# Optimization experiments

Measured on AMD Instinct MI355X. Metric: run time of the kernel, lower is better.

The kernel has to match this reference:

```python
import jax, jax.numpy as jnp
import numpy as np

THR = 0.2          # config['thr']
BORDER = 2         # config['border_rm']
H0C, W0C = 60, 80  # coarse grid of image0 (L = 4800)
H1C, W1C = 60, 80  # coarse grid of image1 (S = 4800)
TEMP_INIT = 10.0


def _border_mask():
    # valid (non-border) positions of the [h0,w0,h1,w1] grid, flattened to [L,S]
    def ok(n):
        a = jnp.arange(n)
        return (a >= BORDER) & (a < n - BORDER)
    m = (ok(H0C)[:, None, None, None] & ok(W0C)[None, :, None, None]
         & ok(H1C)[None, None, :, None] & ok(W1C)[None, None, None, :])
    return m.reshape(H0C * W0C, H1C * W1C)


def setup_inputs() -> dict:
    key = jax.random.key(0)
    k0, k1 = jax.random.split(key)
    feat_c0 = jax.random.normal(k0, (2, 4800, 256), dtype=jnp.float32)
    feat_c1 = jax.random.normal(k1, (2, 4800, 256), dtype=jnp.float32)
    temperature = jnp.asarray(TEMP_INIT, dtype=jnp.float32)
    return {"feat_c0": feat_c0, "feat_c1": feat_c1, "temperature": temperature}


def reference(feat_c0, feat_c1, temperature):
    C = feat_c0.shape[-1]
    inv_sqrt_c = 1.0 / float(C) ** 0.5
    f0 = feat_c0 * inv_sqrt_c
    f1 = feat_c1 * inv_sqrt_c
    # dense similarity GEMM: [N,L,S]
    sim = jnp.einsum('nlc,nsc->nls', f0, f1) * temperature
    # dual softmax -> confidence matrix
    conf = jax.nn.softmax(sim, axis=1) * jax.nn.softmax(sim, axis=2)
    # threshold + border removal (mask_border with b=BORDER)
    mask = (conf > THR) & _border_mask()[None]
    # mutual nearest neighbor
    mutual = (mask
              & (conf == conf.max(axis=2, keepdims=True))
              & (conf == conf.max(axis=1, keepdims=True)))
    # dense mconf map: conf at selected matches, 0 elsewhere (fixed-shape
    # equivalent of the b_ids/i_ids/j_ids nonzero extraction)
    mconf = jnp.where(mutual, conf, jnp.zeros((), conf.dtype))
    return conf, mconf
```

## Files before the change

kernel.cpp:

```cpp
#include <hip/hip_runtime.h>

#define L 4800
#define CH 256
#define NB 2
#define TT 38

typedef float f32x4 __attribute__((ext_vector_type(4)));
typedef _Float16 h16;
typedef _Float16 h16x4 __attribute__((ext_vector_type(4)));
typedef _Float16 h16x8 __attribute__((ext_vector_type(8)));

__global__ __launch_bounds__(256) void convert_init(
    const float* __restrict__ f0, const float* __restrict__ f1,
    h16* __restrict__ A, h16* __restrict__ B,
    float* __restrict__ rowsum, float* __restrict__ colsum,
    unsigned* __restrict__ colmax, unsigned* __restrict__ cand_cnt)
{
    int idx = blockIdx.x * 256 + threadIdx.x;
    if (idx < NB * L) { rowsum[idx] = 0.f; colsum[idx] = 0.f; colmax[idx] = 0u; }
    if (idx == 0) cand_cnt[0] = 0u;
    if (idx >= NB * L * CH / 4) return;
    f32x4 a = ((const f32x4*)f0)[idx];
    f32x4 b = ((const f32x4*)f1)[idx];
    h16x4 ah, bh;
#pragma unroll
    for (int k = 0; k < 4; ++k) { ah[k] = (h16)a[k]; bh[k] = (h16)b[k]; }
    ((h16x4*)A)[idx] = ah;
    ((h16x4*)B)[idx] = bh;
}

__global__ __launch_bounds__(256) void gemm_exp(
    const h16* __restrict__ A, const h16* __restrict__ B,
    const float* __restrict__ temp,
    h16* __restrict__ E, float* __restrict__ rowsum, float* __restrict__ colsum)
{
    __shared__ __align__(16) h16 As[128 * 32];
    __shared__ __align__(16) h16 Bs[128 * 32];
    int bid = blockIdx.x;
    int n = bid / (TT * TT);
    int t = bid % (TT * TT);
    int tm = (t / TT) * 128;
    int tn = (t % TT) * 128;
    const h16* Ab = A + (long)n * L * CH;
    const h16* Bb = B + (long)n * L * CH;
    int tid = threadIdx.x;
    int lane = tid & 63;
    int w = tid >> 6;
    int wr = (w >> 1) * 64;
    int wc = (w & 1) * 64;

    f32x4 acc[4][4] = {};

    int lrow = lane >> 2;
    int kc8 = (lane & 3) * 8;

    for (int k0 = 0; k0 < CH; k0 += 32) {
        __syncthreads();
#pragma unroll
        for (int j = 0; j < 2; ++j) {
            int c = w * 2 + j;
            int row = c * 16 + lrow;
            int ga = tm + row; ga = ga > L - 1 ? L - 1 : ga;
            int gb = tn + row; gb = gb > L - 1 ? L - 1 : gb;
            __builtin_amdgcn_global_load_lds(
                (const __attribute__((address_space(1))) void*)(Ab + (long)ga * CH + k0 + kc8),
                (__attribute__((address_space(3))) void*)(As + c * 512), 16, 0, 0);
            __builtin_amdgcn_global_load_lds(
                (const __attribute__((address_space(1))) void*)(Bb + (long)gb * CH + k0 + kc8),
                (__attribute__((address_space(3))) void*)(Bs + c * 512), 16, 0, 0);
        }
        __syncthreads();

        h16x8 af[4], bf[4];
        int klo = (lane >> 4) * 8;
        int ra = wr + (lane & 15);
        int rb = wc + (lane & 15);
#pragma unroll
        for (int m = 0; m < 4; ++m) af[m] = *(const h16x8*)&As[(ra + m * 16) * 32 + klo];
#pragma unroll
        for (int nf = 0; nf < 4; ++nf) bf[nf] = *(const h16x8*)&Bs[(rb + nf * 16) * 32 + klo];
#pragma unroll
        for (int m = 0; m < 4; ++m)
#pragma unroll
            for (int nf = 0; nf < 4; ++nf)
                acc[m][nf] = __builtin_amdgcn_mfma_f32_16x16x32_f16(af[m], bf[nf], acc[m][nf], 0, 0, 0);
    }

    float scale = temp[0] * (1.0f / 256.0f);
    float rpart[4][4];
#pragma unroll
    for (int m = 0; m < 4; ++m)
#pragma unroll
        for (int j = 0; j < 4; ++j) rpart[m][j] = 0.f;
    float cpart[4] = {0.f, 0.f, 0.f, 0.f};
    int row0 = tm + wr + ((lane >> 4) * 4);
    int col0 = tn + wc + (lane & 15);
#pragma unroll
    for (int m = 0; m < 4; ++m) {
#pragma unroll
        for (int nf = 0; nf < 4; ++nf) {
#pragma unroll
            for (int j = 0; j < 4; ++j) {
                int rr = row0 + m * 16 + j;
                int cc = col0 + nf * 16;
                float e = 0.f;
                if (rr < L && cc < L) {
                    e = __expf(acc[m][nf][j] * scale);
                    E[((long)n * L + rr) * L + cc] = (h16)e;
                }
                rpart[m][j] += e;
                cpart[nf] += e;
            }
        }
    }
#pragma unroll
    for (int m = 0; m < 4; ++m)
#pragma unroll
        for (int j = 0; j < 4; ++j) {
            float v = rpart[m][j];
            v += __shfl_xor(v, 1); v += __shfl_xor(v, 2);
            v += __shfl_xor(v, 4); v += __shfl_xor(v, 8);
            if ((lane & 15) == 0) {
                int rr = row0 + m * 16 + j;
                if (rr < L) atomicAdd(&rowsum[n * L + rr], v);
            }
        }
#pragma unroll
    for (int nf = 0; nf < 4; ++nf) {
        float v = cpart[nf];
        v += __shfl_xor(v, 16); v += __shfl_xor(v, 32);
        if ((lane >> 4) == 0) {
            int cc = col0 + nf * 16;
            if (cc < L) atomicAdd(&colsum[n * L + cc], v);
        }
    }
}

__global__ void inv_kernel(const float* rowsum, const float* colsum, float* inv_rs, float* inv_cs) {
    int i = blockIdx.x * 256 + threadIdx.x;
    if (i < NB * L) { inv_rs[i] = 1.0f / rowsum[i]; inv_cs[i] = 1.0f / colsum[i]; }
}

__global__ __launch_bounds__(256) void conf_row(
    const h16* __restrict__ E, const float* __restrict__ inv_rs, const float* __restrict__ inv_cs,
    float* __restrict__ conf, float* __restrict__ rowmax,
    float* __restrict__ mzero,
    unsigned* __restrict__ cand, unsigned* __restrict__ cand_cnt, unsigned cand_cap)
{
    int b = blockIdx.x;
    int n = b / L;
    const h16x8* E8 = (const h16x8*)(E + (long)b * L);
    const f32x4* IC4 = (const f32x4*)(inv_cs + n * L);
    float* Crow = conf + (long)b * L;
    float irs = inv_rs[b];
    int tid = threadIdx.x;
    float m = 0.f;
    for (int i = tid; i < L / 8; i += 256) {
        h16x8 e8 = E8[i];
        f32x4 ic0 = IC4[2 * i], ic1 = IC4[2 * i + 1];
        f32x4 c0, c1;
#pragma unroll
        for (int k = 0; k < 4; ++k) {
            float e = (float)e8[k];
            float tt = (e * e) * irs;
            c0[k] = tt * ic0[k];
            m = fmaxf(m, c0[k]);
        }
#pragma unroll
        for (int k = 0; k < 4; ++k) {
            float e = (float)e8[4 + k];
            float tt = (e * e) * irs;
            c1[k] = tt * ic1[k];
            m = fmaxf(m, c1[k]);
        }
        *(f32x4*)&Crow[i * 8] = c0;
        *(f32x4*)&Crow[i * 8 + 4] = c1;
#pragma unroll
        for (int k = 0; k < 4; ++k) {
            if (c0[k] > 0.2f) {
                unsigned pos = atomicAdd(cand_cnt, 1u);
                if (pos < cand_cap) cand[pos] = (unsigned)b * L + (unsigned)(i * 8 + k);
            }
            if (c1[k] > 0.2f) {
                unsigned pos = atomicAdd(cand_cnt, 1u);
                if (pos < cand_cap) cand[pos] = (unsigned)b * L + (unsigned)(i * 8 + 4 + k);
            }
        }
    }
    if (mzero) {
        f32x4* M4 = (f32x4*)(mzero + (long)b * L);
        f32x4 z = {0.f, 0.f, 0.f, 0.f};
        for (int i = tid; i < L / 4; i += 256) M4[i] = z;
    }
#pragma unroll
    for (int off = 1; off < 64; off <<= 1) m = fmaxf(m, __shfl_xor(m, off));
    __shared__ float sm[4];
    int lane = tid & 63, wv = tid >> 6;
    if (lane == 0) sm[wv] = m;
    __syncthreads();
    if (tid == 0) rowmax[b] = fmaxf(fmaxf(sm[0], sm[1]), fmaxf(sm[2], sm[3]));
}

__global__ __launch_bounds__(256) void col_max(
    const h16* __restrict__ E, const float* __restrict__ inv_rs, const float* __restrict__ inv_cs,
    unsigned* __restrict__ colmax)
{
    int bx = blockIdx.x;
    int rc = bx & 31;
    int cc = (bx >> 5) % 19;
    int n = bx / (19 * 32);
    int col = cc * 256 + threadIdx.x;
    if (col >= L) return;
    const h16* p = E + ((long)n * L + rc * 150) * L + col;
    const float* irs = inv_rs + n * L + rc * 150;
    float m = 0.f;
    for (int i = 0; i < 150; ++i) {
        float e = (float)(*p);
        float tt = (e * e) * irs[i];
        m = fmaxf(m, tt);
        p += L;
    }
    float v = m * inv_cs[n * L + col];
    atomicMax(&colmax[n * L + col], __float_as_uint(v));
}

__global__ __launch_bounds__(256) void fill_zero(f32x4* __restrict__ p, long n4) {
    long i = (long)blockIdx.x * 256 + threadIdx.x;
    long stride = (long)gridDim.x * 256;
    f32x4 z = {0.f, 0.f, 0.f, 0.f};
    for (; i < n4; i += stride) p[i] = z;
}

__global__ __launch_bounds__(256) void cand_kernel(
    const unsigned* __restrict__ cand_cnt, const unsigned* __restrict__ cand, unsigned cand_cap,
    const float* __restrict__ conf, const float* __restrict__ rowmax,
    const unsigned* __restrict__ colmax, float* __restrict__ mconf)
{
    unsigned cnt = cand_cnt[0];
    if (cnt > cand_cap) cnt = cand_cap;
    for (unsigned i = blockIdx.x * 256 + threadIdx.x; i < cnt; i += gridDim.x * 256) {
        unsigned idx = cand[i];
        unsigned b = idx / L, s = idx % L;
        unsigned n = b / L, l = b % L;
        int h0 = l / 80, w0 = l % 80;
        int h1 = s / 80, w1 = s % 80;
        bool ok = (h0 >= 2) && (h0 < 58) && (w0 >= 2) && (w0 < 78)
               && (h1 >= 2) && (h1 < 58) && (w1 >= 2) && (w1 < 78);
        float c = conf[idx];
        if (ok && c == rowmax[b] && c == __uint_as_float(colmax[n * L + s]))
            mconf[idx] = c;
    }
}

extern "C" void kernel_launch(void* const* d_in, const int* in_sizes, int n_in,
                              void* d_out, int out_size, void* d_ws, size_t ws_size,
                              hipStream_t stream)
{
    const float* f0 = (const float*)d_in[0];
    const float* f1 = (const float*)d_in[1];
    const float* temp = (const float*)d_in[2];

    float* conf  = (float*)d_out;
    float* mconf = conf + (long)NB * L * L;

    h16* Abf = (h16*)d_out;
    h16* Bbf = (h16*)((char*)d_out + 8u * 1024u * 1024u);

    float* rowsum = (float*)d_ws;
    float* colsum = rowsum + NB * L;
    float* inv_rs = colsum + NB * L;
    float* inv_cs = inv_rs + NB * L;
    float* rowmax = inv_cs + NB * L;
    unsigned* colmax = (unsigned*)(rowmax + NB * L);
    unsigned* cand_cnt = colmax + NB * L;
    unsigned* cand = cand_cnt + 1;
    const unsigned cand_cap = 1u << 20;
    size_t stats_end = (size_t)((char*)(cand + cand_cap) - (char*)d_ws);
    size_t E_off = (stats_end + 255) & ~(size_t)255;
    size_t E_bytes = (size_t)NB * L * L * 2;
    bool E_in_ws = ws_size >= E_off + E_bytes;
    h16* E = E_in_ws ? (h16*)((char*)d_ws + E_off) : (h16*)mconf;

    convert_init<<<(NB * L * CH / 4 + 255) / 256, 256, 0, stream>>>(
        f0, f1, Abf, Bbf, rowsum, colsum, colmax, cand_cnt);
    gemm_exp<<<NB * TT * TT, 256, 0, stream>>>(Abf, Bbf, temp, E, rowsum, colsum);
    inv_kernel<<<(NB * L + 255) / 256, 256, 0, stream>>>(rowsum, colsum, inv_rs, inv_cs);
    conf_row<<<NB * L, 256, 0, stream>>>(E, inv_rs, inv_cs, conf, rowmax,
                                         E_in_ws ? mconf : (float*)nullptr,
                                         cand, cand_cnt, cand_cap);
    col_max<<<NB * 19 * 32, 256, 0, stream>>>(E, inv_rs, inv_cs, colmax);
    if (!E_in_ws)
        fill_zero<<<2048, 256, 0, stream>>>((f32x4*)mconf, (long)NB * L * L / 4);
    cand_kernel<<<128, 256, 0, stream>>>(cand_cnt, cand, cand_cap, conf, rowmax, colmax, mconf);
}
```

Baseline: 531.8 us.

## Recompute GEMM in a second pass instead of storing and rereading exp matrix

Replaces the materialized fp16 exp matrix with two GEMM passes. The first computes only row and column exp sums into per-tile partials, with no atomics. The second recomputes the GEMM, writes conf directly, zeroes mconf, and records per-tile row and column maxima. A row-skipping mconf kernel replaces the candidate list and atomics. This trades extra GEMM compute for removing a large intermediate write and read plus the separate column-max scan.

```diff
diff --git a/kernel.cpp b/kernel.cpp
--- a/kernel.cpp
+++ b/kernel.cpp
@@ -4,21 +4,19 @@
 #define CH 256
 #define NB 2
 #define TT 38
+#define NBL (NB * L)
+#define THRF 0.2f
 
 typedef float f32x4 __attribute__((ext_vector_type(4)));
 typedef _Float16 h16;
 typedef _Float16 h16x4 __attribute__((ext_vector_type(4)));
 typedef _Float16 h16x8 __attribute__((ext_vector_type(8)));
 
-__global__ __launch_bounds__(256) void convert_init(
+__global__ __launch_bounds__(256) void convert_kernel(
     const float* __restrict__ f0, const float* __restrict__ f1,
-    h16* __restrict__ A, h16* __restrict__ B,
-    float* __restrict__ rowsum, float* __restrict__ colsum,
-    unsigned* __restrict__ colmax, unsigned* __restrict__ cand_cnt)
+    h16* __restrict__ A, h16* __restrict__ B)
 {
     int idx = blockIdx.x * 256 + threadIdx.x;
-    if (idx < NB * L) { rowsum[idx] = 0.f; colsum[idx] = 0.f; colmax[idx] = 0u; }
-    if (idx == 0) cand_cnt[0] = 0u;
     if (idx >= NB * L * CH / 4) return;
     f32x4 a = ((const f32x4*)f0)[idx];
     f32x4 b = ((const f32x4*)f1)[idx];
@@ -29,13 +27,15 @@
     ((h16x4*)B)[idx] = bh;
 }
 
-__global__ __launch_bounds__(256) void gemm_exp(
+__global__ __launch_bounds__(256) void gemm_pass1(
     const h16* __restrict__ A, const h16* __restrict__ B,
     const float* __restrict__ temp,
-    h16* __restrict__ E, float* __restrict__ rowsum, float* __restrict__ colsum)
+    float* __restrict__ rs_part, float* __restrict__ cs_part)
 {
     __shared__ __align__(16) h16 As[128 * 32];
     __shared__ __align__(16) h16 Bs[128 * 32];
+    __shared__ float rp_lds[128][2];
+    __shared__ float cp_lds[128][2];
     int bid = blockIdx.x;
     int n = bid / (TT * TT);
     int t = bid % (TT * TT);
@@ -50,7 +50,6 @@
     int wc = (w & 1) * 64;
 
     f32x4 acc[4][4] = {};
-
     int lrow = lane >> 2;
     int kc8 = (lane & 3) * 8;
 
@@ -96,23 +95,18 @@
     int row0 = tm + wr + ((lane >> 4) * 4);
     int col0 = tn + wc + (lane & 15);
 #pragma unroll
-    for (int m = 0; m < 4; ++m) {
-#pragma unroll
-        for (int nf = 0; nf < 4; ++nf) {
+    for (int m = 0; m < 4; ++m)
+#pragma unroll
+        for (int nf = 0; nf < 4; ++nf)
 #pragma unroll
             for (int j = 0; j < 4; ++j) {
                 int rr = row0 + m * 16 + j;
                 int cc = col0 + nf * 16;
                 float e = 0.f;
-                if (rr < L && cc < L) {
-                    e = __expf(acc[m][nf][j] * scale);
-                    E[((long)n * L + rr) * L + cc] = (h16)e;
-                }
+                if (rr < L && cc < L) e = __expf(acc[m][nf][j] * scale);
                 rpart[m][j] += e;
                 cpart[nf] += e;
             }
-        }
-    }
 #pragma unroll
     for (int m = 0; m < 4; ++m)
 #pragma unroll
@@ -120,135 +114,204 @@
             float v = rpart[m][j];
             v += __shfl_xor(v, 1); v += __shfl_xor(v, 2);
             v += __shfl_xor(v, 4); v += __shfl_xor(v, 8);
-            if ((lane & 15) == 0) {
-                int rr = row0 + m * 16 + j;
-                if (rr < L) atomicAdd(&rowsum[n * L + rr], v);
-            }
+            if ((lane & 15) == 0)
+                rp_lds[wr + (lane >> 4) * 4 + m * 16 + j][w & 1] = v;
         }
 #pragma unroll
     for (int nf = 0; nf < 4; ++nf) {
         float v = cpart[nf];
         v += __shfl_xor(v, 16); v += __shfl_xor(v, 32);
-        if ((lane >> 4) == 0) {
-            int cc = col0 + nf * 16;
-            if (cc < L) atomicAdd(&colsum[n * L + cc], v);
-        }
-    }
-}
-
-__global__ void inv_kernel(const float* rowsum, const float* colsum, float* inv_rs, float* inv_cs) {
+        if (lane < 16)
+            cp_lds[wc + lane + nf * 16][w >> 1] = v;
+    }
+    __syncthreads();
+    if (tid < 128) {
+        int rr = tm + tid;
+        if (rr < L)
+            rs_part[(long)(t % TT) * NBL + n * L + rr] = rp_lds[tid][0] + rp_lds[tid][1];
+    } else {
+        int c2 = tid - 128;
+        int cc = tn + c2;
+        if (cc < L)
+            cs_part[(long)(t / TT) * NBL + n * L + cc] = cp_lds[c2][0] + cp_lds[c2][1];
+    }
+}
+
+__global__ __launch_bounds__(256) void reduce_inv(
+    const float* __restrict__ rs_part, const float* __restrict__ cs_part,
+    float* __restrict__ inv_rs, float* __restrict__ inv_cs)
+{
     int i = blockIdx.x * 256 + threadIdx.x;
-    if (i < NB * L) { inv_rs[i] = 1.0f / rowsum[i]; inv_cs[i] = 1.0f / colsum[i]; }
-}
-
-__global__ __launch_bounds__(256) void conf_row(
-    const h16* __restrict__ E, const float* __restrict__ inv_rs, const float* __restrict__ inv_cs,
-    float* __restrict__ conf, float* __restrict__ rowmax,
-    float* __restrict__ mzero,
-    unsigned* __restrict__ cand, unsigned* __restrict__ cand_cnt, unsigned cand_cap)
+    if (i < NBL) {
+        float s = 0.f;
+        for (int t = 0; t < TT; ++t) s += rs_part[(long)t * NBL + i];
+        inv_rs[i] = 1.0f / s;
+    } else if (i < 2 * NBL) {
+        int b = i - NBL;
+        float s = 0.f;
+        for (int t = 0; t < TT; ++t) s += cs_part[(long)t * NBL + b];
+        inv_cs[b] = 1.0f / s;
+    }
+}
+
+__global__ __launch_bounds__(256) void gemm_pass2(
+    const h16* __restrict__ A, const h16* __restrict__ B,
+    const float* __restrict__ temp,
+    const float* __restrict__ inv_rs, const float* __restrict__ inv_cs,
+    float* __restrict__ conf, float* __restrict__ mconf,
+    float* __restrict__ rm_part, float* __restrict__ cm_part)
+{
+    __shared__ __align__(16) h16 As[128 * 32];
+    __shared__ __align__(16) h16 Bs[128 * 32];
+    __shared__ float rp_lds[128][2];
+    __shared__ float cp_lds[128][2];
+    int bid = blockIdx.x;
+    int n = bid / (TT * TT);
+    int t = bid % (TT * TT);
+    int tm = (t / TT) * 128;
+    int tn = (t % TT) * 128;
+    const h16* Ab = A + (long)n * L * CH;
+    const h16* Bb = B + (long)n * L * CH;
+    int tid = threadIdx.x;
+    int lane = tid & 63;
+    int w = tid >> 6;
+    int wr = (w >> 1) * 64;
+    int wc = (w & 1) * 64;
+
+    f32x4 acc[4][4] = {};
+    int lrow = lane >> 2;
+    int kc8 = (lane & 3) * 8;
+
+    for (int k0 = 0; k0 < CH; k0 += 32) {
+        __syncthreads();
+#pragma unroll
+        for (int j = 0; j < 2; ++j) {
+            int c = w * 2 + j;
+            int row = c * 16 + lrow;
+            int ga = tm + row; ga = ga > L - 1 ? L - 1 : ga;
+            int gb = tn + row; gb = gb > L - 1 ? L - 1 : gb;
+            __builtin_amdgcn_global_load_lds(
+                (const __attribute__((address_space(1))) void*)(Ab + (long)ga * CH + k0 + kc8),
+                (__attribute__((address_space(3))) void*)(As + c * 512), 16, 0, 0);
+            __builtin_amdgcn_global_load_lds(
+                (const __attribute__((address_space(1))) void*)(Bb + (long)gb * CH + k0 + kc8),
+                (__attribute__((address_space(3))) void*)(Bs + c * 512), 16, 0, 0);
+        }
+        __syncthreads();
+
+        h16x8 af[4], bf[4];
+        int klo = (lane >> 4) * 8;
+        int ra = wr + (lane & 15);
+        int rb = wc + (lane & 15);
+#pragma unroll
+        for (int m = 0; m < 4; ++m) af[m] = *(const h16x8*)&As[(ra + m * 16) * 32 + klo];
+#pragma unroll
+        for (int nf = 0; nf < 4; ++nf) bf[nf] = *(const h16x8*)&Bs[(rb + nf * 16) * 32 + klo];
+#pragma unroll
+        for (int m = 0; m < 4; ++m)
+#pragma unroll
+            for (int nf = 0; nf < 4; ++nf)
+                acc[m][nf] = __builtin_amdgcn_mfma_f32_16x16x32_f16(af[m], bf[nf], acc[m][nf], 0, 0, 0);
+    }
+
+    float scale = temp[0] * (1.0f / 256.0f);
+    int row0 = tm + wr + ((lane >> 4) * 4);
+    int col0 = tn + wc + (lane & 15);
+    float ics[4];
+#pragma unroll
+    for (int nf = 0; nf < 4; ++nf) {
+        int cc = col0 + nf * 16;
+        ics[nf] = (cc < L) ? inv_cs[n * L + cc] : 0.f;
+    }
+    float cmax[4] = {0.f, 0.f, 0.f, 0.f};
+#pragma unroll
+    for (int m = 0; m < 4; ++m)
+#pragma unroll
+        for (int j = 0; j < 4; ++j) {
+            int rr = row0 + m * 16 + j;
+            float irs_v = (rr < L) ? inv_rs[n * L + rr] : 0.f;
+            float rm = 0.f;
+#pragma unroll
+            for (int nf = 0; nf < 4; ++nf) {
+                int cc = col0 + nf * 16;
+                if (rr < L && cc < L) {
+                    float e = __expf(acc[m][nf][j] * scale);
+                    float c = (e * e) * irs_v * ics[nf];
+                    conf[((long)n * L + rr) * L + cc] = c;
+                    rm = fmaxf(rm, c);
+                    cmax[nf] = fmaxf(cmax[nf], c);
+                }
+            }
+            rm = fmaxf(rm, __shfl_xor(rm, 1)); rm = fmaxf(rm, __shfl_xor(rm, 2));
+            rm = fmaxf(rm, __shfl_xor(rm, 4)); rm = fmaxf(rm, __shfl_xor(rm, 8));
+            if ((lane & 15) == 0)
+                rp_lds[wr + (lane >> 4) * 4 + m * 16 + j][w & 1] = rm;
+        }
+#pragma unroll
+    for (int nf = 0; nf < 4; ++nf) {
+        float v = cmax[nf];
+        v = fmaxf(v, __shfl_xor(v, 16)); v = fmaxf(v, __shfl_xor(v, 32));
+        if (lane < 16)
+            cp_lds[wc + lane + nf * 16][w >> 1] = v;
+    }
+    __syncthreads();
+    if (tid < 128) {
+        int rr = tm + tid;
+        if (rr < L)
+            rm_part[(long)(t % TT) * NBL + n * L + rr] = fmaxf(rp_lds[tid][0], rp_lds[tid][1]);
+    } else {
+        int c2 = tid - 128;
+        int cc = tn + c2;
+        if (cc < L)
+            cm_part[(long)(t / TT) * NBL + n * L + cc] = fmaxf(cp_lds[c2][0], cp_lds[c2][1]);
+    }
+
+    f32x4 z = {0.f, 0.f, 0.f, 0.f};
+    for (int i = tid; i < 128 * 32; i += 256) {
+        int r = i >> 5;
+        int cv = (i & 31) * 4;
+        int rr = tm + r, cc = tn + cv;
+        if (rr < L && cc + 3 < L)
+            *(f32x4*)&mconf[((long)n * L + rr) * L + cc] = z;
+    }
+}
+
+__global__ __launch_bounds__(256) void reduce_max(
+    const float* __restrict__ rm_part, const float* __restrict__ cm_part,
+    float* __restrict__ rowmaxf, float* __restrict__ colmaxf)
+{
+    int i = blockIdx.x * 256 + threadIdx.x;
+    if (i < NBL) {
+        float m = 0.f;
+        for (int t = 0; t < TT; ++t) m = fmaxf(m, rm_part[(long)t * NBL + i]);
+        rowmaxf[i] = m;
+    } else if (i < 2 * NBL) {
+        int b = i - NBL;
+        float m = 0.f;
+        for (int t = 0; t < TT; ++t) m = fmaxf(m, cm_part[(long)t * NBL + b]);
+        colmaxf[b] = m;
+    }
+}
+
+__global__ __launch_bounds__(256) void mconf_rows(
+    const float* __restrict__ conf, const float* __restrict__ rowmaxf,
+    const float* __restrict__ colmaxf, float* __restrict__ mconf)
 {
     int b = blockIdx.x;
+    float rmax = rowmaxf[b];
+    if (!(rmax > THRF)) return;
+    int l = b % L;
+    int h0 = l / 80, w0 = l % 80;
+    if (!((h0 >= 2) && (h0 < 58) && (w0 >= 2) && (w0 < 78))) return;
     int n = b / L;
-    const h16x8* E8 = (const h16x8*)(E + (long)b * L);
-    const f32x4* IC4 = (const f32x4*)(inv_cs + n * L);
-    float* Crow = conf + (long)b * L;
-    float irs = inv_rs[b];
-    int tid = threadIdx.x;
-    float m = 0.f;
-    for (int i = tid; i < L / 8; i += 256) {
-        h16x8 e8 = E8[i];
-        f32x4 ic0 = IC4[2 * i], ic1 = IC4[2 * i + 1];
-        f32x4 c0, c1;
-#pragma unroll
-        for (int k = 0; k < 4; ++k) {
-            float e = (float)e8[k];
-            float tt = (e * e) * irs;
-            c0[k] = tt * ic0[k];
-            m = fmaxf(m, c0[k]);
-        }
-#pragma unroll
-        for (int k = 0; k < 4; ++k) {
-            float e = (float)e8[4 + k];
-            float tt = (e * e) * irs;
-            c1[k] = tt * ic1[k];
-            m = fmaxf(m, c1[k]);
-        }
-        *(f32x4*)&Crow[i * 8] = c0;
-        *(f32x4*)&Crow[i * 8 + 4] = c1;
-#pragma unroll
-        for (int k = 0; k < 4; ++k) {
-            if (c0[k] > 0.2f) {
-                unsigned pos = atomicAdd(cand_cnt, 1u);
-                if (pos < cand_cap) cand[pos] = (unsigned)b * L + (unsigned)(i * 8 + k);
-            }
-            if (c1[k] > 0.2f) {
-                unsigned pos = atomicAdd(cand_cnt, 1u);
-                if (pos < cand_cap) cand[pos] = (unsigned)b * L + (unsigned)(i * 8 + 4 + k);
-            }
-        }
-    }
-    if (mzero) {
-        f32x4* M4 = (f32x4*)(mzero + (long)b * L);
-        f32x4 z = {0.f, 0.f, 0.f, 0.f};
-        for (int i = tid; i < L / 4; i += 256) M4[i] = z;
-    }
-#pragma unroll
-    for (int off = 1; off < 64; off <<= 1) m = fmaxf(m, __shfl_xor(m, off));
-    __shared__ float sm[4];
-    int lane = tid & 63, wv = tid >> 6;
-    if (lane == 0) sm[wv] = m;
-    __syncthreads();
-    if (tid == 0) rowmax[b] = fmaxf(fmaxf(sm[0], sm[1]), fmaxf(sm[2], sm[3]));
-}
-
-__global__ __launch_bounds__(256) void col_max(
-    const h16* __restrict__ E, const float* __restrict__ inv_rs, const float* __restrict__ inv_cs,
-    unsigned* __restrict__ colmax)
-{
-    int bx = blockIdx.x;
-    int rc = bx & 31;
-    int cc = (bx >> 5) % 19;
-    int n = bx / (19 * 32);
-    int col = cc * 256 + threadIdx.x;
-    if (col >= L) return;
-    const h16* p = E + ((long)n * L + rc * 150) * L + col;
-    const float* irs = inv_rs + n * L + rc * 150;
-    float m = 0.f;
-    for (int i = 0; i < 150; ++i) {
-        float e = (float)(*p);
-        float tt = (e * e) * irs[i];
-        m = fmaxf(m, tt);
-        p += L;
-    }
-    float v = m * inv_cs[n * L + col];
-    atomicMax(&colmax[n * L + col], __float_as_uint(v));
-}
-
-__global__ __launch_bounds__(256) void fill_zero(f32x4* __restrict__ p, long n4) {
-    long i = (long)blockIdx.x * 256 + threadIdx.x;
-    long stride = (long)gridDim.x * 256;
-    f32x4 z = {0.f, 0.f, 0.f, 0.f};
-    for (; i < n4; i += stride) p[i] = z;
-}
-
-__global__ __launch_bounds__(256) void cand_kernel(
-    const unsigned* __restrict__ cand_cnt, const unsigned* __restrict__ cand, unsigned cand_cap,
-    const float* __restrict__ conf, const float* __restrict__ rowmax,
-    const unsigned* __restrict__ colmax, float* __restrict__ mconf)
-{
-    unsigned cnt = cand_cnt[0];
-    if (cnt > cand_cap) cnt = cand_cap;
-    for (unsigned i = blockIdx.x * 256 + threadIdx.x; i < cnt; i += gridDim.x * 256) {
-        unsigned idx = cand[i];
-        unsigned b = idx / L, s = idx % L;
-        unsigned n = b / L, l = b % L;
-        int h0 = l / 80, w0 = l % 80;
-        int h1 = s / 80, w1 = s % 80;
-        bool ok = (h0 >= 2) && (h0 < 58) && (w0 >= 2) && (w0 < 78)
-               && (h1 >= 2) && (h1 < 58) && (w1 >= 2) && (w1 < 78);
-        float c = conf[idx];
-        if (ok && c == rowmax[b] && c == __uint_as_float(colmax[n * L + s]))
-            mconf[idx] = c;
+    const float* Crow = conf + (long)b * L;
+    for (int s = threadIdx.x; s < L; s += 256) {
+        float c = Crow[s];
+        if (c > THRF && c == rmax && c == colmaxf[n * L + s]) {
+            int h1 = s / 80, w1 = s % 80;
+            if ((h1 >= 2) && (h1 < 58) && (w1 >= 2) && (w1 < 78))
+                mconf[(long)b * L + s] = c;
+        }
     }
 }
 
@@ -263,33 +326,22 @@
     float* conf  = (float*)d_out;
     float* mconf = conf + (long)NB * L * L;
 
-    h16* Abf = (h16*)d_out;
-    h16* Bbf = (h16*)((char*)d_out + 8u * 1024u * 1024u);
-
-    float* rowsum = (float*)d_ws;
-    float* colsum = rowsum + NB * L;
-    float* inv_rs = colsum + NB * L;
-    float* inv_cs = inv_rs + NB * L;
-    float* rowmax = inv_cs + NB * L;
-    unsigned* colmax = (unsigned*)(rowmax + NB * L);
-    unsigned* cand_cnt = colmax + NB * L;
-    unsigned* cand = cand_cnt + 1;
-    const unsigned cand_cap = 1u << 20;
-    size_t stats_end = (size_t)((char*)(cand + cand_cap) - (char*)d_ws);
-    size_t E_off = (stats_end + 255) & ~(size_t)255;
-    size_t E_bytes = (size_t)NB * L * L * 2;
-    bool E_in_ws = ws_size >= E_off + E_bytes;
-    h16* E = E_in_ws ? (h16*)((char*)d_ws + E_off) : (h16*)mconf;
-
-    convert_init<<<(NB * L * CH / 4 + 255) / 256, 256, 0, stream>>>(
-        f0, f1, Abf, Bbf, rowsum, colsum, colmax, cand_cnt);
-    gemm_exp<<<NB * TT * TT, 256, 0, stream>>>(Abf, Bbf, temp, E, rowsum, colsum);
-    inv_kernel<<<(NB * L + 255) / 256, 256, 0, stream>>>(rowsum, colsum, inv_rs, inv_cs);
-    conf_row<<<NB * L, 256, 0, stream>>>(E, inv_rs, inv_cs, conf, rowmax,
-                                         E_in_ws ? mconf : (float*)nullptr,
-                                         cand, cand_cnt, cand_cap);
-    col_max<<<NB * 19 * 32, 256, 0, stream>>>(E, inv_rs, inv_cs, colmax);
-    if (!E_in_ws)
-        fill_zero<<<2048, 256, 0, stream>>>((f32x4*)mconf, (long)NB * L * L / 4);
-    cand_kernel<<<128, 256, 0, stream>>>(cand_cnt, cand, cand_cap, conf, rowmax, colmax, mconf);
-}
+    float* inv_rs  = (float*)d_ws;
+    float* inv_cs  = inv_rs + NBL;
+    float* rowmaxf = inv_cs + NBL;
+    float* colmaxf = rowmaxf + NBL;
+    float* rs_part = colmaxf + NBL;
+    float* cs_part = rs_part + (long)TT * NBL;
+    float* rm_part = cs_part + (long)TT * NBL;
+    float* cm_part = rm_part + (long)TT * NBL;
+    h16*   Abf     = (h16*)(cm_part + (long)TT * NBL);
+    h16*   Bbf     = Abf + (long)NB * L * CH;
+
+    convert_kernel<<<(NB * L * CH / 4 + 255) / 256, 256, 0, stream>>>(f0, f1, Abf, Bbf);
+    gemm_pass1<<<NB * TT * TT, 256, 0, stream>>>(Abf, Bbf, temp, rs_part, cs_part);
+    reduce_inv<<<(2 * NBL + 255) / 256, 256, 0, stream>>>(rs_part, cs_part, inv_rs, inv_cs);
+    gemm_pass2<<<NB * TT * TT, 256, 0, stream>>>(Abf, Bbf, temp, inv_rs, inv_cs,
+                                                 conf, mconf, rm_part, cm_part);
+    reduce_max<<<(2 * NBL + 255) / 256, 256, 0, stream>>>(rm_part, cm_part, rowmaxf, colmaxf);
+    mconf_rows<<<NBL, 256, 0, stream>>>(conf, rowmaxf, colmaxf, mconf);
+}
```

Result: faster. 475.2 us (-10.6%).
